# Performance work log

Hardware: AMD Instinct MI355X
Metric: run time of the kernel (lower is better)

## Reference

```python
import jax, jax.numpy as jnp
import numpy as np

B, F, H, D, TE, CE = 16384, 1024, 64, 256, 4, 4

def setup_inputs() -> dict:
    key = jax.random.key(0)
    ks = iter(jax.random.split(key, 40))
    s = 0.02
    mk = lambda shape: jax.random.normal(next(ks), shape, jnp.float32) * s
    inp = {
        'x_A': jax.random.normal(next(ks), (B, F), jnp.float32),
        'x_S': jax.random.normal(next(ks), (B, F), jnp.float32),
        'x_B': jax.random.normal(next(ks), (B, F), jnp.float32),
        # stacked per-expert weights for the three expert groups (A, Shared, B)
        'W1A': mk((TE, F, H)), 'b1A': mk((TE, H)), 'W2A': mk((TE, H, D)), 'b2A': mk((TE, D)),
        'W1S': mk((CE, F, H)), 'b1S': mk((CE, H)), 'W2S': mk((CE, H, D)), 'b2S': mk((CE, D)),
        'W1B': mk((TE, F, H)), 'b1B': mk((TE, H)), 'W2B': mk((TE, H, D)), 'b2B': mk((TE, D)),
        # gate weights
        'WgA': mk((F, TE + CE)), 'bgA': mk((TE + CE,)),
        'WgB': mk((F, TE + CE)), 'bgB': mk((TE + CE,)),
        'WgS': mk((F, 2 * TE + CE)), 'bgS': mk((2 * TE + CE,)),
    }
    return inp

def _expert_group(x, W1, b1, W2, b2):
    # x: [B,F], W1: [E,F,H] -> [B,E,H]; W2: [E,H,D] -> [B,E,D]
    h = jax.nn.relu(jnp.einsum('bf,efh->beh', x, W1) + b1)  # dropout p=0 -> identity
    return jax.nn.relu(jnp.einsum('beh,ehd->bed', h, W2) + b2)

def reference(x_A, x_S, x_B,
              W1A, b1A, W2A, b2A,
              W1S, b1S, W2S, b2S,
              W1B, b1B, W2B, b2B,
              WgA, bgA, WgB, bgB, WgS, bgS):
    EA = _expert_group(x_A, W1A, b1A, W2A, b2A)  # [B,TE,D]
    ES = _expert_group(x_S, W1S, b1S, W2S, b2S)  # [B,CE,D]
    EB = _expert_group(x_B, W1B, b1B, W2B, b2B)  # [B,TE,D]
    gA = jax.nn.softmax(x_A @ WgA + bgA, axis=1)  # [B,TE+CE]
    gS = jax.nn.softmax(x_S @ WgS + bgS, axis=1)  # [B,2TE+CE]
    gB = jax.nn.softmax(x_B @ WgB + bgB, axis=1)  # [B,TE+CE]
    outA = jnp.einsum('bed,be->bd', jnp.concatenate([EA, ES], axis=1), gA)
    outS = jnp.einsum('bed,be->bd', jnp.concatenate([EA, ES, EB], axis=1), gS)
    outB = jnp.einsum('bed,be->bd', jnp.concatenate([EB, ES], axis=1), gB)
    return (outA, outS, outB)
```

## Files before the change

kernel.cpp:

```cpp
#include <hip/hip_runtime.h>


#define BB 16384
#define FF 1024

typedef _Float16 f16;
typedef __fp16 h16x2 __attribute__((ext_vector_type(2)));
typedef _Float16 f16x8 __attribute__((ext_vector_type(8)));
typedef float f32x4 __attribute__((ext_vector_type(4)));

__device__ __forceinline__ void load_lds16(const void* g, void* l) {
    __builtin_amdgcn_global_load_lds(
        (const __attribute__((address_space(1))) unsigned int*)g,
        (__attribute__((address_space(3))) unsigned int*)l, 16, 0, 0);
}

__device__ __forceinline__ f16x8 pack8(float4 lo, float4 hi) {
    union { f16x8 v; h16x2 p[4]; } u;
    u.p[0] = __builtin_amdgcn_cvt_pkrtz(lo.x, lo.y);
    u.p[1] = __builtin_amdgcn_cvt_pkrtz(lo.z, lo.w);
    u.p[2] = __builtin_amdgcn_cvt_pkrtz(hi.x, hi.y);
    u.p[3] = __builtin_amdgcn_cvt_pkrtz(hi.z, hi.w);
    return u.v;
}

__global__ __launch_bounds__(256) void pack_kernel(
    const float* __restrict__ W1A, const float* __restrict__ W1S, const float* __restrict__ W1B,
    const float* __restrict__ W2A, const float* __restrict__ W2S, const float* __restrict__ W2B,
    const float* __restrict__ WgA, const float* __restrict__ WgS, const float* __restrict__ WgB,
    f16* __restrict__ Wp, f16* __restrict__ W2T, f16* __restrict__ Gp)
{
    int idx = blockIdx.x * 256 + threadIdx.x;
    if (idx < 786432) {
        int g = idx / 262144, rem = idx % 262144;
        int c = rem >> 10, k = rem & 1023;
        const float* W1 = (g == 0) ? W1A : ((g == 1) ? W1S : W1B);
        Wp[idx] = (f16)W1[((c >> 6) << 16) + k * 64 + (c & 63)];
    } else if (idx < 983040) {
        int j = idx - 786432;
        int g = j / 65536, rem = j % 65536;
        int e = rem >> 14, rr = rem & 16383;
        int d = rr >> 6, hh = rr & 63;
        const float* W2 = (g == 0) ? W2A : ((g == 1) ? W2S : W2B);
        W2T[j] = (f16)W2[e * 16384 + hh * 256 + d];
    } else {
        int j = idx - 983040;
        int g = j / 16384, rem = j % 16384;
        int k = rem >> 4, c = rem & 15;
        int ng = (g == 1) ? 12 : 8;
        const float* Wg = (g == 0) ? WgA : ((g == 1) ? WgS : WgB);
        Gp[j] = (c < ng) ? (f16)Wg[k * ng + c] : (f16)0.0f;
    }
}

__global__ __launch_bounds__(256) void l1_kernel(
    const float* __restrict__ xA, const float* __restrict__ xS, const float* __restrict__ xB,
    const float* __restrict__ b1A, const float* __restrict__ b1S, const float* __restrict__ b1B,
    const float* __restrict__ bgA, const float* __restrict__ bgS, const float* __restrict__ bgB,
    const f16* __restrict__ Wp,
    const f16* __restrict__ Gp,
    f16* __restrict__ hbuf,
    float* __restrict__ gates)
{
    const int g = blockIdx.z;
    const float* x  = (g == 0) ? xA  : ((g == 1) ? xS  : xB);
    const float* b1 = (g == 0) ? b1A : ((g == 1) ? b1S : b1B);
    const float* bg = (g == 0) ? bgA : ((g == 1) ? bgS : bgB);
    const int ng = (g == 1) ? 12 : 8;
    float* gout = gates + ((g == 0) ? (size_t)0
                         : (g == 1) ? (size_t)BB * 8
                                    : (size_t)BB * 8 + (size_t)BB * 12);

    const int row0 = blockIdx.y * 128;
    const int col0 = blockIdx.x * 128;
    const bool do_gate = (blockIdx.x == 0);

    __shared__ __align__(16) float Asf[2][128 * 32];
    __shared__ __align__(16) f16   Bsh[2][128 * 32];
    __shared__ __align__(16) f16   Gs[2][16 * 40];

    const int tid  = threadIdx.x;
    const int lane = tid & 63;
    const int wave = tid >> 6;
    const int wm = (wave >> 1) * 64;
    const int wn = (wave & 1) * 64;
    const int lrow = lane & 15;
    const int quad = lane >> 4;

    const f16* Wgrp = Wp + (size_t)g * 256 * 1024;
    const f16* Ggrp = Gp + (size_t)g * 1024 * 16;

    f32x4 acc[4][4] = {};
    f32x4 gacc[4] = {};
    const bool my_gate = do_gate && ((wave & 1) == 0);

    auto stage_gate = [&](int k0, int buf) {
        if (do_gate) {
#pragma unroll
            for (int r = 0; r < 2; ++r) {
                int idx = r * 256 + tid;
                int k = idx >> 4, c = idx & 15;
                Gs[buf][c * 40 + k] = Ggrp[(size_t)(k0 + k) * 16 + c];
            }
        }
    };
    auto stage_ab = [&](int k0, int buf) {
#pragma unroll
        for (int r = 0; r < 4; ++r) {
            int s = r * 256 + tid;
            int m = s >> 3, slot = s & 7;
            int seg = slot ^ (m & 7);
            load_lds16(x + (size_t)(row0 + m) * FF + k0 + seg * 4, &Asf[buf][s * 4]);
        }
#pragma unroll
        for (int r = 0; r < 2; ++r) {
            int s = r * 256 + tid;
            int m = s >> 2, slot = s & 3;
            int seg = slot ^ ((m >> 1) & 3);
            load_lds16(Wgrp + (size_t)(col0 + m) * FF + k0 + seg * 8, &Bsh[buf][s * 8]);
        }
    };

    stage_gate(0, 0);
    __builtin_amdgcn_sched_barrier(0);
    stage_ab(0, 0);
    __builtin_amdgcn_sched_barrier(0);

    for (int t = 0; t < 32; ++t) {
        const int cur = t & 1;
        if (t < 31) {
            stage_gate((t + 1) * 32, cur ^ 1);
            __builtin_amdgcn_sched_barrier(0);
            stage_ab((t + 1) * 32, cur ^ 1);
            __builtin_amdgcn_sched_barrier(0);
            asm volatile("s_waitcnt vmcnt(6) lgkmcnt(0)" ::: "memory");
        } else {
            asm volatile("s_waitcnt vmcnt(0) lgkmcnt(0)" ::: "memory");
        }
        __builtin_amdgcn_sched_barrier(0);
        __builtin_amdgcn_s_barrier();
        __builtin_amdgcn_sched_barrier(0);

        f16x8 af[4], bfr[4];
#pragma unroll
        for (int i = 0; i < 4; ++i) {
            int m = wm + i * 16 + lrow;
            const float* rp = &Asf[cur][m * 32];
            int s0 = (2 * quad) ^ (m & 7);
            int s1 = s0 ^ 1;
            float4 lo = *(const float4*)(rp + s0 * 4);
            float4 hi = *(const float4*)(rp + s1 * 4);
            af[i] = pack8(lo, hi);
        }
#pragma unroll
        for (int j = 0; j < 4; ++j) {
            int n = wn + j * 16 + lrow;
            int slot = quad ^ ((n >> 1) & 3);
            bfr[j] = *(const f16x8*)(&Bsh[cur][n * 32 + slot * 8]);
        }
#pragma unroll
        for (int i = 0; i < 4; ++i)
#pragma unroll
            for (int j = 0; j < 4; ++j)
                acc[i][j] = __builtin_amdgcn_mfma_f32_16x16x32_f16(af[i], bfr[j], acc[i][j], 0, 0, 0);
        if (my_gate) {
            f16x8 gb = *(const f16x8*)(&Gs[cur][lrow * 40 + quad * 8]);
#pragma unroll
            for (int i = 0; i < 4; ++i)
                gacc[i] = __builtin_amdgcn_mfma_f32_16x16x32_f16(af[i], gb, gacc[i], 0, 0, 0);
        }
        asm volatile("s_waitcnt lgkmcnt(0)" ::: "memory");
        __builtin_amdgcn_sched_barrier(0);
        __builtin_amdgcn_s_barrier();
        __builtin_amdgcn_sched_barrier(0);
    }

#pragma unroll
    for (int j = 0; j < 4; ++j) {
        int c = col0 + wn + j * 16 + lrow;
        float bias = b1[c];
#pragma unroll
        for (int i = 0; i < 4; ++i) {
#pragma unroll
            for (int r = 0; r < 4; ++r) {
                int row = row0 + wm + i * 16 + quad * 4 + r;
                float v = fmaxf(acc[i][j][r] + bias, 0.0f);
                hbuf[((size_t)g * BB + row) * 256 + c] = (f16)v;
            }
        }
    }

    if (my_gate) {
        int c = lrow;
        bool valid = (c < ng);
        float bias = valid ? bg[c] : 0.0f;
#pragma unroll
        for (int i = 0; i < 4; ++i) {
#pragma unroll
            for (int r = 0; r < 4; ++r) {
                int row = row0 + wm + i * 16 + quad * 4 + r;
                float logit = valid ? (gacc[i][r] + bias) : -1e30f;
                float mx = logit;
#pragma unroll
                for (int m = 1; m < 16; m <<= 1)
                    mx = fmaxf(mx, __shfl_xor(mx, m, 16));
                float ev = valid ? __expf(logit - mx) : 0.0f;
                float sum = ev;
#pragma unroll
                for (int m = 1; m < 16; m <<= 1)
                    sum += __shfl_xor(sum, m, 16);
                if (valid) gout[(size_t)row * ng + c] = ev / sum;
            }
        }
    }
}

__global__ __launch_bounds__(256) void l2_kernel(
    const f16* __restrict__ hbuf,
    const f16* __restrict__ W2T,
    const float* __restrict__ b2A, const float* __restrict__ b2S, const float* __restrict__ b2B,
    const float* __restrict__ gates,
    float* __restrict__ out)
{
    const int o = blockIdx.y;
    const int row0 = blockIdx.x * 64;
    const int tid = threadIdx.x;
    const int lane = tid & 63;
    const int wave = tid >> 6;
    const int wn = wave * 64;
    const int lrow = lane & 15;
    const int quad = lane >> 4;

    const int ng = (o == 1) ? 12 : 8;
    const float* gp = gates + ((o == 0) ? (size_t)0
                             : (o == 1) ? (size_t)BB * 8
                                        : (size_t)BB * 8 + (size_t)BB * 12);

    __shared__ __align__(16) f16 Ash[2][64 * 64];
    __shared__ __align__(16) f16 Bsh[256 * 64];
    __shared__ float gsh[64 * 12];

    auto group_of = [&](int k) -> int {
        if (o == 0)      return (k < 4) ? 0 : 1;
        else if (o == 1) return k >> 2;
        else             return (k < 4) ? 2 : 1;
    };

    auto stage_h = [&](int k, int buf) {
        int gi = group_of(k), e = k & 3;
        const f16* hs = hbuf + ((size_t)gi * BB + row0) * 256 + e * 64;
#pragma unroll
        for (int r = 0; r < 2; ++r) {
            int s = r * 256 + tid;
            int m = s >> 3, slot = s & 7;
            int seg = slot ^ (m & 7);
            load_lds16(hs + (size_t)m * 256 + seg * 8, &Ash[buf][s * 8]);
        }
    };
    auto stage_w2 = [&](int k) {
        int gi = group_of(k), e = k & 3;
        const f16* w2 = W2T + (size_t)(gi * 4 + e) * 256 * 64;
#pragma unroll
        for (int r = 0; r < 8; ++r) {
            int s = r * 256 + tid;
            int m = s >> 3, slot = s & 7;
            int seg = slot ^ (m & 7);
            load_lds16(w2 + (size_t)m * 64 + seg * 8, &Bsh[s * 8]);
        }
    };

    for (int idx = tid; idx < 64 * ng; idx += 256)
        gsh[idx] = gp[(size_t)(row0 + idx / ng) * ng + (idx % ng)];
    __builtin_amdgcn_sched_barrier(0);
    stage_h(0, 0);
    __builtin_amdgcn_sched_barrier(0);

    f32x4 oacc[4][4] = {};

    for (int k = 0; k < ng; ++k) {
        const int cur = k & 1;
        const int gi = group_of(k), e = k & 3;
        const float* b2 = (gi == 0) ? b2A : ((gi == 1) ? b2S : b2B);

        float bias4[4];
#pragma unroll
        for (int j = 0; j < 4; ++j)
            bias4[j] = b2[e * 256 + wn + j * 16 + lrow];
        __builtin_amdgcn_sched_barrier(0);

        stage_w2(k);
        __builtin_amdgcn_sched_barrier(0);
        if (k + 1 < ng) {
            stage_h(k + 1, cur ^ 1);
            __builtin_amdgcn_sched_barrier(0);
            asm volatile("s_waitcnt vmcnt(2) lgkmcnt(0)" ::: "memory");
        } else {
            asm volatile("s_waitcnt vmcnt(0) lgkmcnt(0)" ::: "memory");
        }
        __builtin_amdgcn_sched_barrier(0);
        __builtin_amdgcn_s_barrier();
        __builtin_amdgcn_sched_barrier(0);

        f32x4 eacc[4][4] = {};
#pragma unroll
        for (int kk = 0; kk < 2; ++kk) {
            f16x8 af[4], bfr[4];
#pragma unroll
            for (int i = 0; i < 4; ++i) {
                int rr = i * 16 + lrow;
                int slot = (kk * 4 + quad) ^ (rr & 7);
                af[i] = *(const f16x8*)(&Ash[cur][rr * 64 + slot * 8]);
            }
#pragma unroll
            for (int j = 0; j < 4; ++j) {
                int n = wn + j * 16 + lrow;
                int slot = (kk * 4 + quad) ^ (n & 7);
                bfr[j] = *(const f16x8*)(&Bsh[n * 64 + slot * 8]);
            }
#pragma unroll
            for (int i = 0; i < 4; ++i)
#pragma unroll
                for (int j = 0; j < 4; ++j)
                    eacc[i][j] = __builtin_amdgcn_mfma_f32_16x16x32_f16(af[i], bfr[j], eacc[i][j], 0, 0, 0);
        }

#pragma unroll
        for (int j = 0; j < 4; ++j) {
            float bias = bias4[j];
#pragma unroll
            for (int i = 0; i < 4; ++i) {
#pragma unroll
                for (int r = 0; r < 4; ++r) {
                    int rl = i * 16 + quad * 4 + r;
                    float v = fmaxf(eacc[i][j][r] + bias, 0.0f);
                    oacc[i][j][r] += gsh[rl * ng + k] * v;
                }
            }
        }
        asm volatile("s_waitcnt lgkmcnt(0)" ::: "memory");
        __builtin_amdgcn_sched_barrier(0);
        __builtin_amdgcn_s_barrier();
        __builtin_amdgcn_sched_barrier(0);
    }

#pragma unroll
    for (int j = 0; j < 4; ++j) {
        int d = wn + j * 16 + lrow;
#pragma unroll
        for (int i = 0; i < 4; ++i) {
#pragma unroll
            for (int r = 0; r < 4; ++r) {
                int rl = i * 16 + quad * 4 + r;
                out[((size_t)o * BB + row0 + rl) * 256 + d] = oacc[i][j][r];
            }
        }
    }
}

extern "C" void kernel_launch(void* const* d_in, const int* in_sizes, int n_in,
                              void* d_out, int out_size, void* d_ws, size_t ws_size,
                              hipStream_t stream)
{
    (void)in_sizes; (void)n_in; (void)out_size; (void)ws_size;

    const float* xA  = (const float*)d_in[0];
    const float* xS  = (const float*)d_in[1];
    const float* xB  = (const float*)d_in[2];
    const float* W1A = (const float*)d_in[3];
    const float* b1A = (const float*)d_in[4];
    const float* W2A = (const float*)d_in[5];
    const float* b2A = (const float*)d_in[6];
    const float* W1S = (const float*)d_in[7];
    const float* b1S = (const float*)d_in[8];
    const float* W2S = (const float*)d_in[9];
    const float* b2S = (const float*)d_in[10];
    const float* W1B = (const float*)d_in[11];
    const float* b1B = (const float*)d_in[12];
    const float* W2B = (const float*)d_in[13];
    const float* b2B = (const float*)d_in[14];
    const float* WgA = (const float*)d_in[15];
    const float* bgA = (const float*)d_in[16];
    const float* WgB = (const float*)d_in[17];
    const float* bgB = (const float*)d_in[18];
    const float* WgS = (const float*)d_in[19];
    const float* bgS = (const float*)d_in[20];

    char* ws = (char*)d_ws;
    f16*   Wp   = (f16*)(ws);
    f16*   W2T  = (f16*)(ws + 0x180000);
    f16*   Gp   = (f16*)(ws + 0x1E0000);
    f16*   hbuf = (f16*)(ws + 0x200000);
    float* gate = (float*)(ws + 0x200000 + 0x1800000);

    pack_kernel<<<4032, 256, 0, stream>>>(W1A, W1S, W1B, W2A, W2S, W2B,
                                          WgA, WgS, WgB, Wp, W2T, Gp);
    l1_kernel<<<dim3(2, 128, 3), 256, 0, stream>>>(
        xA, xS, xB, b1A, b1S, b1B, bgA, bgS, bgB,
        Wp, Gp, hbuf, gate);
    l2_kernel<<<dim3(256, 3), 256, 0, stream>>>(
        hbuf, W2T, b2A, b2S, b2B, gate, (float*)d_out);
}
```

Before: 348.4 us.

## Fuse layer-1, gating and layer-2 into one kernel keeping hidden activations in LDS

The separate l1 and l2 kernels are merged into one persistent-style kernel. Each 512-thread block owns 64 rows and computes all 256 hidden columns for the three groups in sequence, and it keeps the fp16 hidden activations and softmax gates in shared memory. It then runs the second-layer expert GEMMs and accumulates all three gated outputs at once. This removes the global hbuf and gate round-trips and the second read of x across column blocks. In exchange it needs about 156KB of LDS per block, which allows only one block per CU with 8 waves. The gate weight packing is also transposed to suit the new staging.

```diff
diff --git a/kernel.cpp b/kernel.cpp
--- a/kernel.cpp
+++ b/kernel.cpp
@@ -46,315 +46,316 @@
     } else {
         int j = idx - 983040;
         int g = j / 16384, rem = j % 16384;
-        int k = rem >> 4, c = rem & 15;
+        int c = rem >> 10, k = rem & 1023;
         int ng = (g == 1) ? 12 : 8;
         const float* Wg = (g == 0) ? WgA : ((g == 1) ? WgS : WgB);
         Gp[j] = (c < ng) ? (f16)Wg[k * ng + c] : (f16)0.0f;
     }
 }
 
-__global__ __launch_bounds__(256) void l1_kernel(
+__global__ __launch_bounds__(512, 2) void fused_kernel(
     const float* __restrict__ xA, const float* __restrict__ xS, const float* __restrict__ xB,
     const float* __restrict__ b1A, const float* __restrict__ b1S, const float* __restrict__ b1B,
     const float* __restrict__ bgA, const float* __restrict__ bgS, const float* __restrict__ bgB,
+    const float* __restrict__ b2A, const float* __restrict__ b2S, const float* __restrict__ b2B,
     const f16* __restrict__ Wp,
     const f16* __restrict__ Gp,
-    f16* __restrict__ hbuf,
-    float* __restrict__ gates)
+    const f16* __restrict__ W2T,
+    float* __restrict__ out)
 {
-    const int g = blockIdx.z;
-    const float* x  = (g == 0) ? xA  : ((g == 1) ? xS  : xB);
-    const float* b1 = (g == 0) ? b1A : ((g == 1) ? b1S : b1B);
-    const float* bg = (g == 0) ? bgA : ((g == 1) ? bgS : bgB);
-    const int ng = (g == 1) ? 12 : 8;
-    float* gout = gates + ((g == 0) ? (size_t)0
-                         : (g == 1) ? (size_t)BB * 8
-                                    : (size_t)BB * 8 + (size_t)BB * 12);
-
-    const int row0 = blockIdx.y * 128;
-    const int col0 = blockIdx.x * 128;
-    const bool do_gate = (blockIdx.x == 0);
-
-    __shared__ __align__(16) float Asf[2][128 * 32];
-    __shared__ __align__(16) f16   Bsh[2][128 * 32];
-    __shared__ __align__(16) f16   Gs[2][16 * 40];
+    extern __shared__ char smem[];
+    f16*   hls   = (f16*)smem;
+    char*  stage = smem + 98304;
+    float* Xs    = (float*)stage;
+    f16*   Ws    = (f16*)(stage + 24576);
+    f16*   W2s   = (f16*)stage;
+    float* b2s   = (float*)(stage + 32768);
+    float* gsh   = (float*)(stage + 45056);
+    f16*   Gs    = (f16*)(smem + 157696);
 
     const int tid  = threadIdx.x;
     const int lane = tid & 63;
-    const int wave = tid >> 6;
-    const int wm = (wave >> 1) * 64;
-    const int wn = (wave & 1) * 64;
+    const int w    = tid >> 6;
     const int lrow = lane & 15;
     const int quad = lane >> 4;
-
-    const f16* Wgrp = Wp + (size_t)g * 256 * 1024;
-    const f16* Ggrp = Gp + (size_t)g * 1024 * 16;
-
-    f32x4 acc[4][4] = {};
-    f32x4 gacc[4] = {};
-    const bool my_gate = do_gate && ((wave & 1) == 0);
-
-    auto stage_gate = [&](int k0, int buf) {
-        if (do_gate) {
-#pragma unroll
-            for (int r = 0; r < 2; ++r) {
-                int idx = r * 256 + tid;
-                int k = idx >> 4, c = idx & 15;
-                Gs[buf][c * 40 + k] = Ggrp[(size_t)(k0 + k) * 16 + c];
-            }
-        }
-    };
-    auto stage_ab = [&](int k0, int buf) {
-#pragma unroll
-        for (int r = 0; r < 4; ++r) {
-            int s = r * 256 + tid;
+    const int row0 = blockIdx.x * 64;
+
+    const int wm = (w >> 2) * 32;
+    const int wn = (w & 3) * 64;
+    const int rblk = (w & 3) * 16;
+    const int wn2  = (w >> 2) * 64;
+
+    const bool gate_wave = ((w & 3) == 0);
+
+    float b1vA[4], b1vS[4], b1vB[4];
+#pragma unroll
+    for (int j = 0; j < 4; ++j) {
+        int c = wn + j * 16 + lrow;
+        b1vA[j] = b1A[c]; b1vS[j] = b1S[c]; b1vB[j] = b1B[c];
+    }
+    float bgv0 = (lrow < 8)  ? bgA[lrow] : 0.0f;
+    float bgv1 = (lrow < 12) ? bgS[lrow] : 0.0f;
+    float bgv2 = (lrow < 8)  ? bgB[lrow] : 0.0f;
+
+    auto stage_x = [&](int t) {
+        int g = t >> 5, k0 = (t & 31) * 32;
+        const float* xg = (g == 0) ? xA : ((g == 1) ? xS : xB);
+        int s = tid;
+        int m = s >> 3, slot = s & 7;
+        int seg = slot ^ (m & 7);
+        load_lds16(xg + (size_t)(row0 + m) * FF + k0 + seg * 4,
+                   Xs + (size_t)(t % 3) * 2048 + s * 4);
+    };
+    auto stage_w = [&](int t) {
+        int g = t >> 5, k0 = (t & 31) * 32;
+        const f16* wg = Wp + (size_t)g * 262144;
+#pragma unroll
+        for (int r = 0; r < 2; ++r) {
+            int s = r * 512 + tid;
+            int m = s >> 2, slot = s & 3;
+            int seg = slot ^ ((m >> 1) & 3);
+            load_lds16(wg + (size_t)m * FF + k0 + seg * 8,
+                       Ws + (size_t)(t & 1) * 8192 + s * 8);
+        }
+    };
+    auto stage_g = [&](int t) {
+        int g = t >> 5, k0 = (t & 31) * 32;
+        load_lds16(Gp + (size_t)g * 16384 + (size_t)(lane >> 2) * 1024 + k0 + (lane & 3) * 8,
+                   Gs + (size_t)(t & 1) * 512 + lane * 8);
+    };
+
+    f32x4 acc[2][4] = {};
+    f32x4 gacc[2] = {};
+    f32x4 gsvA[2], gsvS[2], gsvB[2];
+
+    auto h_write = [&](int g, const float (&bv)[4]) {
+        f16* hb = hls + g * 16384;
+#pragma unroll
+        for (int j = 0; j < 4; ++j) {
+            int col = wn + j * 16 + lrow;
+            float bias = bv[j];
+#pragma unroll
+            for (int i = 0; i < 2; ++i)
+#pragma unroll
+                for (int r = 0; r < 4; ++r) {
+                    int row = wm + i * 16 + quad * 4 + r;
+                    float v = fmaxf(acc[i][j][r] + bias, 0.0f);
+                    hb[row * 256 + (col ^ ((row & 7) << 3))] = (f16)v;
+                }
+        }
+    };
+
+    stage_x(0);
+    __builtin_amdgcn_sched_barrier(0);
+    stage_w(0);
+    __builtin_amdgcn_sched_barrier(0);
+    stage_g(0);
+    __builtin_amdgcn_sched_barrier(0);
+    stage_x(1);
+    __builtin_amdgcn_sched_barrier(0);
+
+    for (int t = 0; t < 96; ++t) {
+        int t1 = t + 1;
+        int t2 = t + 2;
+        if (t < 95) {
+            stage_w(t1);
+            __builtin_amdgcn_sched_barrier(0);
+            stage_g(t1);
+            __builtin_amdgcn_sched_barrier(0);
+        }
+        if (t < 94) {
+            stage_x(t2);
+            __builtin_amdgcn_sched_barrier(0);
+        }
+        if (t < 94)      { asm volatile("s_waitcnt vmcnt(5)" ::: "memory"); }
+        else if (t == 94){ asm volatile("s_waitcnt vmcnt(4)" ::: "memory"); }
+        else             { asm volatile("s_waitcnt vmcnt(0)" ::: "memory"); }
+        __builtin_amdgcn_sched_barrier(0);
+        __builtin_amdgcn_s_barrier();
+        __builtin_amdgcn_sched_barrier(0);
+
+        {
+            const float* xb = Xs + (t % 3) * 2048;
+            const f16* wb = Ws + (t & 1) * 8192;
+            f16x8 af[2], bfr[4];
+#pragma unroll
+            for (int i = 0; i < 2; ++i) {
+                int m = wm + i * 16 + lrow;
+                const float* rp = xb + m * 32;
+                int s0 = (2 * quad) ^ (m & 7);
+                float4 lo = *(const float4*)(rp + s0 * 4);
+                float4 hi = *(const float4*)(rp + (s0 ^ 1) * 4);
+                af[i] = pack8(lo, hi);
+            }
+#pragma unroll
+            for (int j = 0; j < 4; ++j) {
+                int n = wn + j * 16 + lrow;
+                int slot = quad ^ ((n >> 1) & 3);
+                bfr[j] = *(const f16x8*)(wb + n * 32 + slot * 8);
+            }
+#pragma unroll
+            for (int i = 0; i < 2; ++i)
+#pragma unroll
+                for (int j = 0; j < 4; ++j)
+                    acc[i][j] = __builtin_amdgcn_mfma_f32_16x16x32_f16(af[i], bfr[j], acc[i][j], 0, 0, 0);
+            if (gate_wave) {
+                f16x8 gb = *(const f16x8*)(Gs + (t & 1) * 512 + lrow * 32 + quad * 8);
+#pragma unroll
+                for (int i = 0; i < 2; ++i)
+                    gacc[i] = __builtin_amdgcn_mfma_f32_16x16x32_f16(af[i], gb, gacc[i], 0, 0, 0);
+            }
+        }
+
+        if ((t & 31) == 31) {
+            int g = t >> 5;
+            if (g == 0)      { h_write(0, b1vA); if (gate_wave) { gsvA[0] = gacc[0]; gsvA[1] = gacc[1]; } }
+            else if (g == 1) { h_write(1, b1vS); if (gate_wave) { gsvS[0] = gacc[0]; gsvS[1] = gacc[1]; } }
+            else             { h_write(2, b1vB); if (gate_wave) { gsvB[0] = gacc[0]; gsvB[1] = gacc[1]; } }
+#pragma unroll
+            for (int i = 0; i < 2; ++i) {
+#pragma unroll
+                for (int j = 0; j < 4; ++j) acc[i][j] = (f32x4){0.f, 0.f, 0.f, 0.f};
+                gacc[i] = (f32x4){0.f, 0.f, 0.f, 0.f};
+            }
+        }
+
+        asm volatile("s_waitcnt lgkmcnt(0)" ::: "memory");
+        __builtin_amdgcn_sched_barrier(0);
+        __builtin_amdgcn_s_barrier();
+        __builtin_amdgcn_sched_barrier(0);
+    }
+
+    auto stage_w2 = [&](int c, int buf) {
+        int p = c >> 1, dh = c & 1;
+        int gi = p >> 2, e = p & 3;
+        const f16* w2 = W2T + (size_t)(gi * 4 + e) * 16384 + (size_t)dh * 8192;
+#pragma unroll
+        for (int r = 0; r < 2; ++r) {
+            int s = r * 512 + tid;
             int m = s >> 3, slot = s & 7;
             int seg = slot ^ (m & 7);
-            load_lds16(x + (size_t)(row0 + m) * FF + k0 + seg * 4, &Asf[buf][s * 4]);
-        }
-#pragma unroll
-        for (int r = 0; r < 2; ++r) {
-            int s = r * 256 + tid;
-            int m = s >> 2, slot = s & 3;
-            int seg = slot ^ ((m >> 1) & 3);
-            load_lds16(Wgrp + (size_t)(col0 + m) * FF + k0 + seg * 8, &Bsh[buf][s * 8]);
-        }
-    };
-
-    stage_gate(0, 0);
-    __builtin_amdgcn_sched_barrier(0);
-    stage_ab(0, 0);
-    __builtin_amdgcn_sched_barrier(0);
-
-    for (int t = 0; t < 32; ++t) {
-        const int cur = t & 1;
-        if (t < 31) {
-            stage_gate((t + 1) * 32, cur ^ 1);
-            __builtin_amdgcn_sched_barrier(0);
-            stage_ab((t + 1) * 32, cur ^ 1);
-            __builtin_amdgcn_sched_barrier(0);
-            asm volatile("s_waitcnt vmcnt(6) lgkmcnt(0)" ::: "memory");
-        } else {
-            asm volatile("s_waitcnt vmcnt(0) lgkmcnt(0)" ::: "memory");
-        }
-        __builtin_amdgcn_sched_barrier(0);
-        __builtin_amdgcn_s_barrier();
-        __builtin_amdgcn_sched_barrier(0);
-
-        f16x8 af[4], bfr[4];
-#pragma unroll
-        for (int i = 0; i < 4; ++i) {
-            int m = wm + i * 16 + lrow;
-            const float* rp = &Asf[cur][m * 32];
-            int s0 = (2 * quad) ^ (m & 7);
-            int s1 = s0 ^ 1;
-            float4 lo = *(const float4*)(rp + s0 * 4);
-            float4 hi = *(const float4*)(rp + s1 * 4);
-            af[i] = pack8(lo, hi);
-        }
+            load_lds16(w2 + (size_t)m * 64 + seg * 8,
+                       W2s + (size_t)buf * 8192 + s * 8);
+        }
+    };
+
+    {
+        const float* s1 = (tid < 256) ? (b2A + tid * 4) : (b2S + (tid - 256) * 4);
+        load_lds16(s1, b2s + tid * 4);
+        __builtin_amdgcn_sched_barrier(0);
+        if (tid < 256) load_lds16(b2B + tid * 4, b2s + 2048 + tid * 4);
+        __builtin_amdgcn_sched_barrier(0);
+    }
+    stage_w2(0, 0);
+    __builtin_amdgcn_sched_barrier(0);
+
+    if (gate_wave) {
+        auto softmax_store = [&](const f32x4 (&gsv)[2], float bgc, int ng, int goff) {
+            int c = lrow;
+            bool valid = (c < ng);
+#pragma unroll
+            for (int i = 0; i < 2; ++i)
+#pragma unroll
+                for (int r = 0; r < 4; ++r) {
+                    int row = wm + i * 16 + quad * 4 + r;
+                    float logit = valid ? (gsv[i][r] + bgc) : -1e30f;
+                    float mx = logit;
+#pragma unroll
+                    for (int m = 1; m < 16; m <<= 1) mx = fmaxf(mx, __shfl_xor(mx, m, 16));
+                    float ev = valid ? __expf(logit - mx) : 0.0f;
+                    float sum = ev;
+#pragma unroll
+                    for (int m = 1; m < 16; m <<= 1) sum += __shfl_xor(sum, m, 16);
+                    if (valid) gsh[row * 28 + goff + c] = ev / sum;
+                }
+        };
+        softmax_store(gsvA, bgv0, 8, 0);
+        softmax_store(gsvS, bgv1, 12, 8);
+        softmax_store(gsvB, bgv2, 8, 20);
+    }
+    asm volatile("s_waitcnt vmcnt(2) lgkmcnt(0)" ::: "memory");
+    __builtin_amdgcn_sched_barrier(0);
+    __builtin_amdgcn_s_barrier();
+    __builtin_amdgcn_sched_barrier(0);
+
+    f32x4 oA[2][4] = {}, oS[2][4] = {}, oB[2][4] = {};
+
+    for (int p = 0; p < 12; ++p) {
+        int gi = p >> 2, e = p & 3;
+#pragma unroll
+        for (int dh = 0; dh < 2; ++dh) {
+            int c = p * 2 + dh;
+            if (c < 23) {
+                stage_w2(c + 1, dh ^ 1);
+                __builtin_amdgcn_sched_barrier(0);
+                asm volatile("s_waitcnt vmcnt(2)" ::: "memory");
+            } else {
+                asm volatile("s_waitcnt vmcnt(0)" ::: "memory");
+            }
+            __builtin_amdgcn_sched_barrier(0);
+            __builtin_amdgcn_s_barrier();
+            __builtin_amdgcn_sched_barrier(0);
+
+            float bias[4];
+#pragma unroll
+            for (int j = 0; j < 4; ++j)
+                bias[j] = b2s[gi * 1024 + e * 256 + dh * 128 + wn2 + j * 16 + lrow];
+
+            const f16* wb = W2s + dh * 8192;
+            f32x4 eacc[4] = {};
+#pragma unroll
+            for (int kk = 0; kk < 2; ++kk) {
+                int row = rblk + lrow;
+                int u = (kk * 32 + quad * 8) ^ ((row & 7) << 3);
+                f16x8 af = *(const f16x8*)(hls + gi * 16384 + row * 256 + e * 64 + u);
+                f16x8 bfr[4];
+#pragma unroll
+                for (int j = 0; j < 4; ++j) {
+                    int n = wn2 + j * 16 + lrow;
+                    int slot = (kk * 4 + quad) ^ (n & 7);
+                    bfr[j] = *(const f16x8*)(wb + n * 64 + slot * 8);
+                }
+#pragma unroll
+                for (int j = 0; j < 4; ++j)
+                    eacc[j] = __builtin_amdgcn_mfma_f32_16x16x32_f16(af, bfr[j], eacc[j], 0, 0, 0);
+            }
+
+#pragma unroll
+            for (int r = 0; r < 4; ++r) {
+                int row = rblk + quad * 4 + r;
+                float ga = 0.f, gs = 0.f, gb = 0.f;
+                if (gi == 0)      { ga = gsh[row * 28 + e];      gs = gsh[row * 28 + 8 + e]; }
+                else if (gi == 1) { ga = gsh[row * 28 + 4 + e];  gs = gsh[row * 28 + 12 + e]; gb = gsh[row * 28 + 24 + e]; }
+                else              { gs = gsh[row * 28 + 16 + e]; gb = gsh[row * 28 + 20 + e]; }
+#pragma unroll
+                for (int j = 0; j < 4; ++j) {
+                    float v = fmaxf(eacc[j][r] + bias[j], 0.0f);
+                    if (gi == 0)      { oA[dh][j][r] += ga * v; oS[dh][j][r] += gs * v; }
+                    else if (gi == 1) { oA[dh][j][r] += ga * v; oS[dh][j][r] += gs * v; oB[dh][j][r] += gb * v; }
+                    else              { oS[dh][j][r] += gs * v; oB[dh][j][r] += gb * v; }
+                }
+            }
+
+            asm volatile("s_waitcnt lgkmcnt(0)" ::: "memory");
+            __builtin_amdgcn_sched_barrier(0);
+            __builtin_amdgcn_s_barrier();
+            __builtin_amdgcn_sched_barrier(0);
+        }
+    }
+
+#pragma unroll
+    for (int dh = 0; dh < 2; ++dh)
 #pragma unroll
         for (int j = 0; j < 4; ++j) {
-            int n = wn + j * 16 + lrow;
-            int slot = quad ^ ((n >> 1) & 3);
-            bfr[j] = *(const f16x8*)(&Bsh[cur][n * 32 + slot * 8]);
-        }
-#pragma unroll
-        for (int i = 0; i < 4; ++i)
-#pragma unroll
-            for (int j = 0; j < 4; ++j)
-                acc[i][j] = __builtin_amdgcn_mfma_f32_16x16x32_f16(af[i], bfr[j], acc[i][j], 0, 0, 0);
-        if (my_gate) {
-            f16x8 gb = *(const f16x8*)(&Gs[cur][lrow * 40 + quad * 8]);
-#pragma unroll
-            for (int i = 0; i < 4; ++i)
-                gacc[i] = __builtin_amdgcn_mfma_f32_16x16x32_f16(af[i], gb, gacc[i], 0, 0, 0);
-        }
-        asm volatile("s_waitcnt lgkmcnt(0)" ::: "memory");
-        __builtin_amdgcn_sched_barrier(0);
-        __builtin_amdgcn_s_barrier();
-        __builtin_amdgcn_sched_barrier(0);
-    }
-
-#pragma unroll
-    for (int j = 0; j < 4; ++j) {
-        int c = col0 + wn + j * 16 + lrow;
-        float bias = b1[c];
-#pragma unroll
-        for (int i = 0; i < 4; ++i) {
+            int d = dh * 128 + wn2 + j * 16 + lrow;
 #pragma unroll
             for (int r = 0; r < 4; ++r) {
-                int row = row0 + wm + i * 16 + quad * 4 + r;
-                float v = fmaxf(acc[i][j][r] + bias, 0.0f);
-                hbuf[((size_t)g * BB + row) * 256 + c] = (f16)v;
-            }
-        }
-    }
-
-    if (my_gate) {
-        int c = lrow;
-        bool valid = (c < ng);
-        float bias = valid ? bg[c] : 0.0f;
-#pragma unroll
-        for (int i = 0; i < 4; ++i) {
-#pragma unroll
-            for (int r = 0; r < 4; ++r) {
-                int row = row0 + wm + i * 16 + quad * 4 + r;
-                float logit = valid ? (gacc[i][r] + bias) : -1e30f;
-                float mx = logit;
-#pragma unroll
-                for (int m = 1; m < 16; m <<= 1)
-                    mx = fmaxf(mx, __shfl_xor(mx, m, 16));
-                float ev = valid ? __expf(logit - mx) : 0.0f;
-                float sum = ev;
-#pragma unroll
-                for (int m = 1; m < 16; m <<= 1)
-                    sum += __shfl_xor(sum, m, 16);
-                if (valid) gout[(size_t)row * ng + c] = ev / sum;
-            }
-        }
-    }
-}
-
-__global__ __launch_bounds__(256) void l2_kernel(
-    const f16* __restrict__ hbuf,
-    const f16* __restrict__ W2T,
-    const float* __restrict__ b2A, const float* __restrict__ b2S, const float* __restrict__ b2B,
-    const float* __restrict__ gates,
-    float* __restrict__ out)
-{
-    const int o = blockIdx.y;
-    const int row0 = blockIdx.x * 64;
-    const int tid = threadIdx.x;
-    const int lane = tid & 63;
-    const int wave = tid >> 6;
-    const int wn = wave * 64;
-    const int lrow = lane & 15;
-    const int quad = lane >> 4;
-
-    const int ng = (o == 1) ? 12 : 8;
-    const float* gp = gates + ((o == 0) ? (size_t)0
-                             : (o == 1) ? (size_t)BB * 8
-                                        : (size_t)BB * 8 + (size_t)BB * 12);
-
-    __shared__ __align__(16) f16 Ash[2][64 * 64];
-    __shared__ __align__(16) f16 Bsh[256 * 64];
-    __shared__ float gsh[64 * 12];
-
-    auto group_of = [&](int k) -> int {
-        if (o == 0)      return (k < 4) ? 0 : 1;
-        else if (o == 1) return k >> 2;
-        else             return (k < 4) ? 2 : 1;
-    };
-
-    auto stage_h = [&](int k, int buf) {
-        int gi = group_of(k), e = k & 3;
-        const f16* hs = hbuf + ((size_t)gi * BB + row0) * 256 + e * 64;
-#pragma unroll
-        for (int r = 0; r < 2; ++r) {
-            int s = r * 256 + tid;
-            int m = s >> 3, slot = s & 7;
-            int seg = slot ^ (m & 7);
-            load_lds16(hs + (size_t)m * 256 + seg * 8, &Ash[buf][s * 8]);
-        }
-    };
-    auto stage_w2 = [&](int k) {
-        int gi = group_of(k), e = k & 3;
-        const f16* w2 = W2T + (size_t)(gi * 4 + e) * 256 * 64;
-#pragma unroll
-        for (int r = 0; r < 8; ++r) {
-            int s = r * 256 + tid;
-            int m = s >> 3, slot = s & 7;
-            int seg = slot ^ (m & 7);
-            load_lds16(w2 + (size_t)m * 64 + seg * 8, &Bsh[s * 8]);
-        }
-    };
-
-    for (int idx = tid; idx < 64 * ng; idx += 256)
-        gsh[idx] = gp[(size_t)(row0 + idx / ng) * ng + (idx % ng)];
-    __builtin_amdgcn_sched_barrier(0);
-    stage_h(0, 0);
-    __builtin_amdgcn_sched_barrier(0);
-
-    f32x4 oacc[4][4] = {};
-
-    for (int k = 0; k < ng; ++k) {
-        const int cur = k & 1;
-        const int gi = group_of(k), e = k & 3;
-        const float* b2 = (gi == 0) ? b2A : ((gi == 1) ? b2S : b2B);
-
-        float bias4[4];
-#pragma unroll
-        for (int j = 0; j < 4; ++j)
-            bias4[j] = b2[e * 256 + wn + j * 16 + lrow];
-        __builtin_amdgcn_sched_barrier(0);
-
-        stage_w2(k);
-        __builtin_amdgcn_sched_barrier(0);
-        if (k + 1 < ng) {
-            stage_h(k + 1, cur ^ 1);
-            __builtin_amdgcn_sched_barrier(0);
-            asm volatile("s_waitcnt vmcnt(2) lgkmcnt(0)" ::: "memory");
-        } else {
-            asm volatile("s_waitcnt vmcnt(0) lgkmcnt(0)" ::: "memory");
-        }
-        __builtin_amdgcn_sched_barrier(0);
-        __builtin_amdgcn_s_barrier();
-        __builtin_amdgcn_sched_barrier(0);
-
-        f32x4 eacc[4][4] = {};
-#pragma unroll
-        for (int kk = 0; kk < 2; ++kk) {
-            f16x8 af[4], bfr[4];
-#pragma unroll
-            for (int i = 0; i < 4; ++i) {
-                int rr = i * 16 + lrow;
-                int slot = (kk * 4 + quad) ^ (rr & 7);
-                af[i] = *(const f16x8*)(&Ash[cur][rr * 64 + slot * 8]);
-            }
-#pragma unroll
-            for (int j = 0; j < 4; ++j) {
-                int n = wn + j * 16 + lrow;
-                int slot = (kk * 4 + quad) ^ (n & 7);
-                bfr[j] = *(const f16x8*)(&Bsh[n * 64 + slot * 8]);
-            }
-#pragma unroll
-            for (int i = 0; i < 4; ++i)
-#pragma unroll
-                for (int j = 0; j < 4; ++j)
-                    eacc[i][j] = __builtin_amdgcn_mfma_f32_16x16x32_f16(af[i], bfr[j], eacc[i][j], 0, 0, 0);
-        }
-
-#pragma unroll
-        for (int j = 0; j < 4; ++j) {
-            float bias = bias4[j];
-#pragma unroll
-            for (int i = 0; i < 4; ++i) {
-#pragma unroll
-                for (int r = 0; r < 4; ++r) {
-                    int rl = i * 16 + quad * 4 + r;
-                    float v = fmaxf(eacc[i][j][r] + bias, 0.0f);
-                    oacc[i][j][r] += gsh[rl * ng + k] * v;
-                }
-            }
-        }
-        asm volatile("s_waitcnt lgkmcnt(0)" ::: "memory");
-        __builtin_amdgcn_sched_barrier(0);
-        __builtin_amdgcn_s_barrier();
-        __builtin_amdgcn_sched_barrier(0);
-    }
-
-#pragma unroll
-    for (int j = 0; j < 4; ++j) {
-        int d = wn + j * 16 + lrow;
-#pragma unroll
-        for (int i = 0; i < 4; ++i) {
-#pragma unroll
-            for (int r = 0; r < 4; ++r) {
-                int rl = i * 16 + quad * 4 + r;
-                out[((size_t)o * BB + row0 + rl) * 256 + d] = oacc[i][j][r];
-            }
-        }
-    }
+                int row = row0 + rblk + quad * 4 + r;
+                out[((size_t)0 * BB + row) * 256 + d] = oA[dh][j][r];
+                out[((size_t)1 * BB + row) * 256 + d] = oS[dh][j][r];
+                out[((size_t)2 * BB + row) * 256 + d] = oB[dh][j][r];
+            }
+        }
 }
 
 extern "C" void kernel_launch(void* const* d_in, const int* in_sizes, int n_in,
@@ -386,17 +387,13 @@
     const float* bgS = (const float*)d_in[20];
 
     char* ws = (char*)d_ws;
-    f16*   Wp   = (f16*)(ws);
-    f16*   W2T  = (f16*)(ws + 0x180000);
-    f16*   Gp   = (f16*)(ws + 0x1E0000);
-    f16*   hbuf = (f16*)(ws + 0x200000);
-    float* gate = (float*)(ws + 0x200000 + 0x1800000);
+    f16* Wp  = (f16*)(ws);
+    f16* W2T = (f16*)(ws + 0x180000);
+    f16* Gp  = (f16*)(ws + 0x1E0000);
 
     pack_kernel<<<4032, 256, 0, stream>>>(W1A, W1S, W1B, W2A, W2S, W2B,
                                           WgA, WgS, WgB, Wp, W2T, Gp);
-    l1_kernel<<<dim3(2, 128, 3), 256, 0, stream>>>(
-        xA, xS, xB, b1A, b1S, b1B, bgA, bgS, bgB,
-        Wp, Gp, hbuf, gate);
-    l2_kernel<<<dim3(256, 3), 256, 0, stream>>>(
-        hbuf, W2T, b2A, b2S, b2B, gate, (float*)d_out);
-}
+    fused_kernel<<<256, 512, 159744, stream>>>(
+        xA, xS, xB, b1A, b1S, b1B, bgA, bgS, bgB, b2A, b2S, b2B,
+        Wp, Gp, W2T, (float*)d_out);
+}
```

Result: slower. 356.1 us (+2.2%).
